# Optimization experiments

Measured on AMD Instinct MI355X. Metric: run time of the kernel, lower is better.

## Reference

```python
import jax, jax.numpy as jnp
import numpy as np

N = 100000   # nodes
E = 1600000  # edges (avg degree 16)
D = 64       # feature / hidden / embedding dim
OUT = 2
NEG_SLOPE = 0.2


def setup_inputs() -> dict:
    key = jax.random.key(0)
    ks = jax.random.split(key, 12)
    s = 1.0 / np.sqrt(D)
    return {
        "x": jax.random.normal(ks[0], (N, D), dtype=jnp.float32),
        "edge_index": jax.random.randint(ks[1], (2, E), 0, N, dtype=jnp.int64),
        "Wl": jax.random.normal(ks[2], (3, D, D), dtype=jnp.float32) * s,
        "bl": jnp.zeros((3, D), dtype=jnp.float32),
        "Wr": jax.random.normal(ks[3], (3, D, D), dtype=jnp.float32) * s,
        "br": jnp.zeros((3, D), dtype=jnp.float32),
        "att": jax.random.normal(ks[4], (3, D), dtype=jnp.float32) * s,
        "bg": jnp.zeros((3, D), dtype=jnp.float32),
        "Ws": jax.random.normal(ks[5], (3, D, D), dtype=jnp.float32) * s,
        "bs": jnp.zeros((3, D), dtype=jnp.float32),
        "Wout": jax.random.normal(ks[6], (D, OUT), dtype=jnp.float32) * s,
        "bout": jnp.zeros((OUT,), dtype=jnp.float32),
    }


def _gatv2(h, src, dst, Wl, bl, Wr, br, att, bg):
    # GATv2Conv (heads=1, concat, add_self_loops=False):
    #   e_ij = att . LeakyReLU(Wl h_j + Wr h_i); softmax over incoming edges of i;
    #   out_i = sum_j alpha_ij * (Wl h_j) + bias
    xl = h @ Wl + bl                      # [N, D] source transform
    xr = h @ Wr + br                      # [N, D] dest transform
    e = jax.nn.leaky_relu(xl[src] + xr[dst], NEG_SLOPE) @ att  # [E]
    m = jax.ops.segment_max(e, dst, num_segments=N)            # per-dest max
    a = jnp.exp(e - m[dst])                                    # [E]
    denom = jax.ops.segment_sum(a, dst, num_segments=N)        # [N]
    alpha = a / denom[dst]                                     # [E]
    agg = jax.ops.segment_sum(alpha[:, None] * xl[src], dst, num_segments=N)
    return agg + bg                                            # [N, D]


def reference(x, edge_index, Wl, bl, Wr, br, att, bg, Ws, bs, Wout, bout):
    src, dst = edge_index[0], edge_index[1]
    # layer 1: gat1 + skip1, relu (dropout_rate=0 -> identity)
    h = jax.nn.relu(_gatv2(x, src, dst, Wl[0], bl[0], Wr[0], br[0], att[0], bg[0])
                    + x @ Ws[0] + bs[0])
    # middle layer
    h = jax.nn.relu(_gatv2(h, src, dst, Wl[1], bl[1], Wr[1], br[1], att[1], bg[1])
                    + h @ Ws[1] + bs[1])
    # last gat layer: no relu after
    h = _gatv2(h, src, dst, Wl[2], bl[2], Wr[2], br[2], att[2], bg[2]) + h @ Ws[2] + bs[2]
    return h @ Wout + bout
```

## Files before the change

kernel.cpp:

```cpp
#include <hip/hip_runtime.h>
#include <stdint.h>

#define NN 100000
#define EE 1600000
#define DD 64
#define NBUCK 391
#define SCWG 200
#define SCCHUNK 8000

using short8 = __attribute__((ext_vector_type(8))) short;
using f32x4  = __attribute__((ext_vector_type(4))) float;
using f2     = __attribute__((ext_vector_type(2))) float;


__device__ __forceinline__ unsigned short bf16_rne(float f) {
    unsigned int u = __float_as_uint(f);
    unsigned int r = (u + 0x7FFFu + ((u >> 16) & 1u)) >> 16;
    return (unsigned short)r;
}
__device__ __forceinline__ float bf16_to_f32(unsigned short h) {
    return __uint_as_float(((unsigned int)h) << 16);
}


__global__ void bucket_hist(const int* __restrict__ dst, int* __restrict__ bhist) {
    __shared__ int h[NBUCK];
    int t = threadIdx.x;
    for (int b = t; b < NBUCK; b += 256) h[b] = 0;
    __syncthreads();
    int start = blockIdx.x * SCCHUNK;
    int endi = min(start + SCCHUNK, EE);
    for (int e = start + t; e < endi; e += 256)
        atomicAdd(&h[dst[e] >> 8], 1);
    __syncthreads();
    for (int b = t; b < NBUCK; b += 256)
        if (h[b]) atomicAdd(&bhist[b], h[b]);
}

__global__ void bucket_scan(const int* __restrict__ bhist, int* __restrict__ bbase,
                            int* __restrict__ bcursor, int* __restrict__ offsets) {
    __shared__ int s[512];
    int t = threadIdx.x;
    int v = (t < NBUCK) ? bhist[t] : 0;
    s[t] = v;
    __syncthreads();
    for (int off = 1; off < 512; off <<= 1) {
        int a = (t >= off) ? s[t - off] : 0;
        __syncthreads();
        s[t] += a;
        __syncthreads();
    }
    if (t < NBUCK) { int excl = s[t] - v; bbase[t] = excl; bcursor[t] = excl; }
    if (t == 0) { bbase[NBUCK] = EE; offsets[NN] = EE; }
}

__global__ void bucket_scatter(const int* __restrict__ src, const int* __restrict__ dst,
                               int* __restrict__ bcursor, unsigned int* __restrict__ bedges) {
    __shared__ int cnt[NBUCK];
    __shared__ int lcur[NBUCK];
    int t = threadIdx.x;
    for (int b = t; b < NBUCK; b += 256) cnt[b] = 0;
    __syncthreads();
    int start = blockIdx.x * SCCHUNK;
    int endi = min(start + SCCHUNK, EE);
    for (int e = start + t; e < endi; e += 256)
        atomicAdd(&cnt[dst[e] >> 8], 1);
    __syncthreads();
    for (int b = t; b < NBUCK; b += 256) {
        int c = cnt[b];
        lcur[b] = c ? atomicAdd(&bcursor[b], c) : 0;
    }
    __syncthreads();
    for (int e = start + t; e < endi; e += 256) {
        int d = dst[e];
        int pos = atomicAdd(&lcur[d >> 8], 1);
        bedges[pos] = ((unsigned int)(d & 255) << 24) | (unsigned int)src[e];
    }
}

__global__ void bucket_csr(const unsigned int* __restrict__ bedges, const int* __restrict__ bbase,
                           int* __restrict__ offsets, int* __restrict__ csr) {
    __shared__ int ncnt[256];
    __shared__ int lofs[256];
    int b = blockIdx.x;
    int t = threadIdx.x;
    int beg = bbase[b], endb = bbase[b + 1];
    ncnt[t] = 0;
    __syncthreads();
    for (int e = beg + t; e < endb; e += 256)
        atomicAdd(&ncnt[bedges[e] >> 24], 1);
    __syncthreads();
    int v = ncnt[t];
    lofs[t] = v;
    __syncthreads();
    for (int off = 1; off < 256; off <<= 1) {
        int a = (t >= off) ? lofs[t - off] : 0;
        __syncthreads();
        lofs[t] += a;
        __syncthreads();
    }
    int excl = lofs[t] - v;
    int node = b * 256 + t;
    if (node < NN) offsets[node] = beg + excl;
    __syncthreads();
    ncnt[t] = beg + excl;
    __syncthreads();
    for (int e = beg + t; e < endb; e += 256) {
        unsigned int ed = bedges[e];
        int pos = atomicAdd(&ncnt[ed >> 24], 1);
        csr[pos] = (int)(ed & 0xFFFFFFu);
    }
}


__global__ void conv_w(const float* __restrict__ Wl, const float* __restrict__ Wr,
                       const float* __restrict__ Ws,
                       unsigned short* __restrict__ Wt_hi, unsigned short* __restrict__ Wt_lo) {
    int e = blockIdx.x * 256 + threadIdx.x;
    if (e >= 9 * 4096) return;
    int mat = e >> 12;
    int r   = e & 4095;
    int k   = r >> 6, n = r & 63;
    int L = mat / 3, j = mat % 3;
    const float* W = (j == 0) ? Wl : ((j == 1) ? Wr : Ws);
    float v = W[L * 4096 + k * 64 + n];
    unsigned short hi = bf16_rne(v);
    unsigned short lo = bf16_rne(v - bf16_to_f32(hi));
    Wt_hi[mat * 4096 + n * 64 + k] = hi;
    Wt_lo[mat * 4096 + n * 64 + k] = lo;
}


__global__ void conv_x(const float* __restrict__ x,
                       unsigned short* __restrict__ Ahi, unsigned short* __restrict__ Alo) {
    int i = blockIdx.x * 256 + threadIdx.x;
    int total = NN * 16;
    for (; i < total; i += gridDim.x * 256) {
        float4 v = *(const float4*)&x[(size_t)i * 4];
        ushort4 h, l;
        h.x = bf16_rne(v.x); l.x = bf16_rne(v.x - bf16_to_f32(h.x));
        h.y = bf16_rne(v.y); l.y = bf16_rne(v.y - bf16_to_f32(h.y));
        h.z = bf16_rne(v.z); l.z = bf16_rne(v.z - bf16_to_f32(h.z));
        h.w = bf16_rne(v.w); l.w = bf16_rne(v.w - bf16_to_f32(h.w));
        *(ushort4*)&Ahi[(size_t)i * 4] = h;
        *(ushort4*)&Alo[(size_t)i * 4] = l;
    }
}


__global__ __launch_bounds__(256) void gemm_mfma(
    const unsigned short* __restrict__ Ahi, const unsigned short* __restrict__ Alo,
    const unsigned short* __restrict__ Wt_hi, const unsigned short* __restrict__ Wt_lo,
    const float* __restrict__ bl, const float* __restrict__ br, const float* __restrict__ bs,
    unsigned short* __restrict__ Xlb, float* __restrict__ XRS) {
    int lane = threadIdx.x & 63;
    int wid  = threadIdx.x >> 6;
    int m0 = (blockIdx.x * 4 + wid) * 16;
    if (m0 >= NN) return;

    int arow = m0 + (lane & 15);
    if (arow >= NN) arow = NN - 1;
    int koff = (lane >> 4) * 8;

    const unsigned short* abase = Ahi + (size_t)arow * 64;
    const unsigned short* lbase = Alo + (size_t)arow * 64;
    short8 ahi0 = *(const short8*)(abase + koff);
    short8 ahi1 = *(const short8*)(abase + 32 + koff);
    short8 alo0 = *(const short8*)(lbase + koff);
    short8 alo1 = *(const short8*)(lbase + 32 + koff);

    int col16 = lane & 15;
    int r0 = m0 + ((lane >> 4) << 2);

#pragma unroll
    for (int m = 0; m < 3; m++) {
        const unsigned short* wh = Wt_hi + m * 4096;
        const unsigned short* wl = Wt_lo + m * 4096;
        const float* bias = (m == 0) ? bl : ((m == 1) ? br : bs);
#pragma unroll
        for (int tt = 0; tt < 4; tt++) {
            int ncol = tt * 16 + col16;
            const unsigned short* bh = wh + ncol * 64 + koff;
            const unsigned short* blo = wl + ncol * 64 + koff;
            short8 bhi0 = *(const short8*)bh;
            short8 bhi1 = *(const short8*)(bh + 32);
            short8 blo0 = *(const short8*)blo;
            short8 blo1 = *(const short8*)(blo + 32);

            f32x4 acc = {0.f, 0.f, 0.f, 0.f};
            acc = __builtin_amdgcn_mfma_f32_16x16x32_bf16(ahi0, bhi0, acc, 0, 0, 0);
            acc = __builtin_amdgcn_mfma_f32_16x16x32_bf16(ahi1, bhi1, acc, 0, 0, 0);
            acc = __builtin_amdgcn_mfma_f32_16x16x32_bf16(ahi0, blo0, acc, 0, 0, 0);
            acc = __builtin_amdgcn_mfma_f32_16x16x32_bf16(ahi1, blo1, acc, 0, 0, 0);
            acc = __builtin_amdgcn_mfma_f32_16x16x32_bf16(alo0, bhi0, acc, 0, 0, 0);
            acc = __builtin_amdgcn_mfma_f32_16x16x32_bf16(alo1, bhi1, acc, 0, 0, 0);

            float bb = bias[ncol];
#pragma unroll
            for (int j = 0; j < 4; j++) {
                int row = r0 + j;
                if (row < NN) {
                    float v = acc[j] + bb;
                    if (m == 0)      Xlb[(size_t)row * 64 + ncol]       = bf16_rne(v);
                    else if (m == 1) XRS[(size_t)row * 128 + ncol]      = v;
                    else             XRS[(size_t)row * 128 + 64 + ncol] = v;
                }
            }
        }
    }
}


__device__ __forceinline__ float group_sum16(float t) {
    t += __int_as_float(__builtin_amdgcn_update_dpp(0, __float_as_int(t), 0xB1, 0xF, 0xF, true));
    t += __int_as_float(__builtin_amdgcn_update_dpp(0, __float_as_int(t), 0x4E, 0xF, 0xF, true));
    t += __int_as_float(__builtin_amdgcn_update_dpp(0, __float_as_int(t), 0x141, 0xF, 0xF, true));
    t += __int_as_float(__builtin_amdgcn_update_dpp(0, __float_as_int(t), 0x140, 0xF, 0xF, true));
    return t;
}

__global__ __launch_bounds__(256) void node_kernel(
    const unsigned short* __restrict__ Xlb, const float* __restrict__ XRS,
    const int* __restrict__ offsets, const int* __restrict__ csr,
    const float* __restrict__ att, const float* __restrict__ bg,
    unsigned short* __restrict__ houtHi, unsigned short* __restrict__ houtLo, int do_relu,
    const float* __restrict__ Wout, const float* __restrict__ bout,
    float* __restrict__ outp, int do_out) {
    int lane = threadIdx.x & 63;
    int wid  = threadIdx.x >> 6;
    int i = blockIdx.x * 4 + wid;
    if (i >= NN) return;
    int sub = lane & 15;
    int grp = lane >> 4;

    float4 xr4  = *(const float4*)&XRS[(size_t)i * 128 + sub * 4];
    float4 att4 = *(const float4*)&att[sub * 4];
    f2 xr01 = {xr4.x, xr4.y}, xr23 = {xr4.z, xr4.w};
    f2 at01 = {att4.x, att4.y}, at23 = {att4.z, att4.w};

    f2 agg01 = {0.f, 0.f}, agg23 = {0.f, 0.f};
    float denom = 0.f;
    int beg = offsets[i], end = offsets[i + 1];

    for (int j0 = beg; j0 < end; j0 += 8) {
        int jA = j0 + grp, jB = j0 + grp + 4;
        bool vA = jA < end, vB = jB < end;
        int sA = csr[vA ? jA : beg];
        int sB = csr[vB ? jB : beg];
        uint2 uA = *(const uint2*)&Xlb[(size_t)sA * 64 + sub * 4];
        uint2 uB = *(const uint2*)&Xlb[(size_t)sB * 64 + sub * 4];
        f2 xA01 = { __uint_as_float(uA.x << 16), __uint_as_float(uA.x & 0xFFFF0000u) };
        f2 xA23 = { __uint_as_float(uA.y << 16), __uint_as_float(uA.y & 0xFFFF0000u) };
        f2 xB01 = { __uint_as_float(uB.x << 16), __uint_as_float(uB.x & 0xFFFF0000u) };
        f2 xB23 = { __uint_as_float(uB.y << 16), __uint_as_float(uB.y & 0xFFFF0000u) };

        f2 sA01 = xA01 + xr01;
        f2 sA23 = xA23 + xr23;
        f2 sB01 = xB01 + xr01;
        f2 sB23 = xB23 + xr23;
        f2 lA01 = { fmaxf(sA01.x, 0.2f * sA01.x), fmaxf(sA01.y, 0.2f * sA01.y) };
        f2 lA23 = { fmaxf(sA23.x, 0.2f * sA23.x), fmaxf(sA23.y, 0.2f * sA23.y) };
        f2 lB01 = { fmaxf(sB01.x, 0.2f * sB01.x), fmaxf(sB01.y, 0.2f * sB01.y) };
        f2 lB23 = { fmaxf(sB23.x, 0.2f * sB23.x), fmaxf(sB23.y, 0.2f * sB23.y) };

        f2 tAv = lA01 * at01 + lA23 * at23;
        f2 tBv = lB01 * at01 + lB23 * at23;
        float tA = group_sum16(tAv.x + tAv.y);
        float tB = group_sum16(tBv.x + tBv.y);
        float aA = vA ? __expf(tA) : 0.f;
        float aB = vB ? __expf(tB) : 0.f;

        f2 aAv = {aA, aA};
        f2 aBv = {aB, aB};
        agg01 += aAv * xA01 + aBv * xB01;
        agg23 += aAv * xA23 + aBv * xB23;
        denom += aA + aB;
    }

    float aggx = agg01.x, aggy = agg01.y, aggz = agg23.x, aggw = agg23.y;
#pragma unroll
    for (int m = 16; m <= 32; m <<= 1) {
        aggx  += __shfl_xor(aggx, m, 64);
        aggy  += __shfl_xor(aggy, m, 64);
        aggz  += __shfl_xor(aggz, m, 64);
        aggw  += __shfl_xor(aggw, m, 64);
        denom += __shfl_xor(denom, m, 64);
    }

    float inv = (denom > 0.f) ? (1.0f / denom) : 0.f;
    float4 sk4 = *(const float4*)&XRS[(size_t)i * 128 + 64 + sub * 4];
    float4 bg4 = *(const float4*)&bg[sub * 4];
    float4 res;
    res.x = aggx * inv + bg4.x + sk4.x;
    res.y = aggy * inv + bg4.y + sk4.y;
    res.z = aggz * inv + bg4.z + sk4.z;
    res.w = aggw * inv + bg4.w + sk4.w;
    if (do_relu) {
        res.x = fmaxf(res.x, 0.f); res.y = fmaxf(res.y, 0.f);
        res.z = fmaxf(res.z, 0.f); res.w = fmaxf(res.w, 0.f);
    }
    if (do_out) {
        float4 w01 = *(const float4*)&Wout[8 * sub];
        float4 w23 = *(const float4*)&Wout[8 * sub + 4];
        float o0 = res.x * w01.x + res.y * w01.z + res.z * w23.x + res.w * w23.z;
        float o1 = res.x * w01.y + res.y * w01.w + res.z * w23.y + res.w * w23.w;
        o0 = group_sum16(o0);
        o1 = group_sum16(o1);
        if (lane == 0) {
            outp[(size_t)i * 2 + 0] = o0 + bout[0];
            outp[(size_t)i * 2 + 1] = o1 + bout[1];
        }
    } else {
        if (grp == 0) {
            ushort4 h, l;
            h.x = bf16_rne(res.x); l.x = bf16_rne(res.x - bf16_to_f32(h.x));
            h.y = bf16_rne(res.y); l.y = bf16_rne(res.y - bf16_to_f32(h.y));
            h.z = bf16_rne(res.z); l.z = bf16_rne(res.z - bf16_to_f32(h.z));
            h.w = bf16_rne(res.w); l.w = bf16_rne(res.w - bf16_to_f32(h.w));
            *(ushort4*)&houtHi[(size_t)i * 64 + sub * 4] = h;
            *(ushort4*)&houtLo[(size_t)i * 64 + sub * 4] = l;
        }
    }
}


extern "C" void kernel_launch(void* const* d_in, const int* in_sizes, int n_in,
                              void* d_out, int out_size, void* d_ws, size_t ws_size,
                              hipStream_t stream) {
    const float* x    = (const float*)d_in[0];
    const int*   ei   = (const int*)d_in[1];
    const float* Wl   = (const float*)d_in[2];
    const float* bl   = (const float*)d_in[3];
    const float* Wr   = (const float*)d_in[4];
    const float* br   = (const float*)d_in[5];
    const float* att  = (const float*)d_in[6];
    const float* bg   = (const float*)d_in[7];
    const float* Ws   = (const float*)d_in[8];
    const float* bs   = (const float*)d_in[9];
    const float* Wout = (const float*)d_in[10];
    const float* bout = (const float*)d_in[11];
    float* out = (float*)d_out;

    size_t off = 0;
    char* base = (char*)d_ws;
    auto alloc = [&](size_t bytes) -> void* {
        void* p = base + off;
        off += (bytes + 255) & ~(size_t)255;
        return p;
    };
    unsigned short* Xlb = (unsigned short*)alloc((size_t)NN * 64 * 2);
    float* XRS  = (float*)alloc((size_t)NN * 128 * 4);
    unsigned short* Ahi = (unsigned short*)alloc((size_t)NN * 64 * 2);
    unsigned short* Alo = (unsigned short*)alloc((size_t)NN * 64 * 2);
    unsigned short* Bhi = (unsigned short*)alloc((size_t)NN * 64 * 2);
    unsigned short* Blo = (unsigned short*)alloc((size_t)NN * 64 * 2);
    unsigned short* Wthi = (unsigned short*)alloc((size_t)9 * 4096 * 2);
    unsigned short* Wtlo = (unsigned short*)alloc((size_t)9 * 4096 * 2);
    int*  bhist  = (int*)alloc((size_t)NBUCK * 4);
    int*  bbase  = (int*)alloc((size_t)(NBUCK + 1) * 4);
    int*  bcur   = (int*)alloc((size_t)NBUCK * 4);
    unsigned int* bedges = (unsigned int*)alloc((size_t)EE * 4);
    int*  offs   = (int*)alloc((size_t)(NN + 1) * 4);
    int*  csr    = (int*)alloc((size_t)EE * 4);

    const int* src = ei;
    const int* dst = ei + EE;

    hipMemsetAsync(bhist, 0, (size_t)NBUCK * 4, stream);
    bucket_hist<<<SCWG, 256, 0, stream>>>(dst, bhist);
    bucket_scan<<<1, 512, 0, stream>>>(bhist, bbase, bcur, offs);
    bucket_scatter<<<SCWG, 256, 0, stream>>>(src, dst, bcur, bedges);
    bucket_csr<<<NBUCK, 256, 0, stream>>>(bedges, bbase, offs, csr);

    conv_w<<<(9 * 4096 + 255) / 256, 256, 0, stream>>>(Wl, Wr, Ws, Wthi, Wtlo);
    conv_x<<<2048, 256, 0, stream>>>(x, Ahi, Alo);

    unsigned short* curHi = Ahi; unsigned short* curLo = Alo;
    unsigned short* nxtHi = Bhi; unsigned short* nxtLo = Blo;
    for (int L = 0; L < 3; L++) {
        gemm_mfma<<<(NN + 63) / 64, 256, 0, stream>>>(
            curHi, curLo, Wthi + (size_t)L * 3 * 4096, Wtlo + (size_t)L * 3 * 4096,
            bl + L * 64, br + L * 64, bs + L * 64, Xlb, XRS);
        node_kernel<<<NN / 4, 256, 0, stream>>>(
            Xlb, XRS, offs, csr, att + L * 64, bg + L * 64,
            nxtHi, nxtLo, (L < 2) ? 1 : 0,
            Wout, bout, out, (L == 2) ? 1 : 0);
        unsigned short* th = curHi; curHi = nxtHi; nxtHi = th;
        unsigned short* tl = curLo; curLo = nxtLo; nxtLo = tl;
    }
}
```

Measured before the change: 382.2 us.

## Merge weight/input conversion kernels, transpose MFMA output for vector stores, use exp2

```diff
diff --git a/kernel.cpp b/kernel.cpp
--- a/kernel.cpp
+++ b/kernel.cpp
@@ -113,37 +113,37 @@
 }
 
 
-__global__ void conv_w(const float* __restrict__ Wl, const float* __restrict__ Wr,
-                       const float* __restrict__ Ws,
-                       unsigned short* __restrict__ Wt_hi, unsigned short* __restrict__ Wt_lo) {
-    int e = blockIdx.x * 256 + threadIdx.x;
-    if (e >= 9 * 4096) return;
-    int mat = e >> 12;
-    int r   = e & 4095;
-    int k   = r >> 6, n = r & 63;
-    int L = mat / 3, j = mat % 3;
-    const float* W = (j == 0) ? Wl : ((j == 1) ? Wr : Ws);
-    float v = W[L * 4096 + k * 64 + n];
-    unsigned short hi = bf16_rne(v);
-    unsigned short lo = bf16_rne(v - bf16_to_f32(hi));
-    Wt_hi[mat * 4096 + n * 64 + k] = hi;
-    Wt_lo[mat * 4096 + n * 64 + k] = lo;
-}
-
-
-__global__ void conv_x(const float* __restrict__ x,
-                       unsigned short* __restrict__ Ahi, unsigned short* __restrict__ Alo) {
-    int i = blockIdx.x * 256 + threadIdx.x;
-    int total = NN * 16;
-    for (; i < total; i += gridDim.x * 256) {
-        float4 v = *(const float4*)&x[(size_t)i * 4];
-        ushort4 h, l;
-        h.x = bf16_rne(v.x); l.x = bf16_rne(v.x - bf16_to_f32(h.x));
-        h.y = bf16_rne(v.y); l.y = bf16_rne(v.y - bf16_to_f32(h.y));
-        h.z = bf16_rne(v.z); l.z = bf16_rne(v.z - bf16_to_f32(h.z));
-        h.w = bf16_rne(v.w); l.w = bf16_rne(v.w - bf16_to_f32(h.w));
-        *(ushort4*)&Ahi[(size_t)i * 4] = h;
-        *(ushort4*)&Alo[(size_t)i * 4] = l;
+__global__ void conv_wx(const float* __restrict__ Wl, const float* __restrict__ Wr,
+                        const float* __restrict__ Ws, const float* __restrict__ x,
+                        unsigned short* __restrict__ Wt_hi, unsigned short* __restrict__ Wt_lo,
+                        unsigned short* __restrict__ Ahi, unsigned short* __restrict__ Alo) {
+    if (blockIdx.x < 144) {
+        int e = blockIdx.x * 256 + threadIdx.x;
+        if (e >= 9 * 4096) return;
+        int mat = e >> 12;
+        int r   = e & 4095;
+        int k   = r >> 6, n = r & 63;
+        int L = mat / 3, j = mat % 3;
+        const float* W = (j == 0) ? Wl : ((j == 1) ? Wr : Ws);
+        float v = W[L * 4096 + k * 64 + n];
+        unsigned short hi = bf16_rne(v);
+        unsigned short lo = bf16_rne(v - bf16_to_f32(hi));
+        Wt_hi[mat * 4096 + n * 64 + k] = hi;
+        Wt_lo[mat * 4096 + n * 64 + k] = lo;
+    } else {
+        int i = (blockIdx.x - 144) * 256 + threadIdx.x;
+        int total = NN * 16;
+        int stride = (gridDim.x - 144) * 256;
+        for (; i < total; i += stride) {
+            float4 v = *(const float4*)&x[(size_t)i * 4];
+            ushort4 h, l;
+            h.x = bf16_rne(v.x); l.x = bf16_rne(v.x - bf16_to_f32(h.x));
+            h.y = bf16_rne(v.y); l.y = bf16_rne(v.y - bf16_to_f32(h.y));
+            h.z = bf16_rne(v.z); l.z = bf16_rne(v.z - bf16_to_f32(h.z));
+            h.w = bf16_rne(v.w); l.w = bf16_rne(v.w - bf16_to_f32(h.w));
+            *(ushort4*)&Ahi[(size_t)i * 4] = h;
+            *(ushort4*)&Alo[(size_t)i * 4] = l;
+        }
     }
 }
 
@@ -158,9 +158,13 @@
     int m0 = (blockIdx.x * 4 + wid) * 16;
     if (m0 >= NN) return;
 
-    int arow = m0 + (lane & 15);
-    if (arow >= NN) arow = NN - 1;
-    int koff = (lane >> 4) * 8;
+    int l4 = lane & 15;
+    int hi = lane >> 4;
+    int koff = hi * 8;
+
+    int arow = m0 + l4;
+    bool rowok = (arow < NN);
+    if (!rowok) arow = NN - 1;
 
     const unsigned short* abase = Ahi + (size_t)arow * 64;
     const unsigned short* lbase = Alo + (size_t)arow * 64;
@@ -169,8 +173,7 @@
     short8 alo0 = *(const short8*)(lbase + koff);
     short8 alo1 = *(const short8*)(lbase + 32 + koff);
 
-    int col16 = lane & 15;
-    int r0 = m0 + ((lane >> 4) << 2);
+    int nbase0 = hi * 4;
 
 #pragma unroll
     for (int m = 0; m < 3; m++) {
@@ -179,7 +182,7 @@
         const float* bias = (m == 0) ? bl : ((m == 1) ? br : bs);
 #pragma unroll
         for (int tt = 0; tt < 4; tt++) {
-            int ncol = tt * 16 + col16;
+            int ncol = tt * 16 + l4;
             const unsigned short* bh = wh + ncol * 64 + koff;
             const unsigned short* blo = wl + ncol * 64 + koff;
             short8 bhi0 = *(const short8*)bh;
@@ -188,22 +191,29 @@
             short8 blo1 = *(const short8*)(blo + 32);
 
             f32x4 acc = {0.f, 0.f, 0.f, 0.f};
-            acc = __builtin_amdgcn_mfma_f32_16x16x32_bf16(ahi0, bhi0, acc, 0, 0, 0);
-            acc = __builtin_amdgcn_mfma_f32_16x16x32_bf16(ahi1, bhi1, acc, 0, 0, 0);
-            acc = __builtin_amdgcn_mfma_f32_16x16x32_bf16(ahi0, blo0, acc, 0, 0, 0);
-            acc = __builtin_amdgcn_mfma_f32_16x16x32_bf16(ahi1, blo1, acc, 0, 0, 0);
-            acc = __builtin_amdgcn_mfma_f32_16x16x32_bf16(alo0, bhi0, acc, 0, 0, 0);
-            acc = __builtin_amdgcn_mfma_f32_16x16x32_bf16(alo1, bhi1, acc, 0, 0, 0);
-
-            float bb = bias[ncol];
-#pragma unroll
-            for (int j = 0; j < 4; j++) {
-                int row = r0 + j;
-                if (row < NN) {
-                    float v = acc[j] + bb;
-                    if (m == 0)      Xlb[(size_t)row * 64 + ncol]       = bf16_rne(v);
-                    else if (m == 1) XRS[(size_t)row * 128 + ncol]      = v;
-                    else             XRS[(size_t)row * 128 + 64 + ncol] = v;
+            acc = __builtin_amdgcn_mfma_f32_16x16x32_bf16(bhi0, ahi0, acc, 0, 0, 0);
+            acc = __builtin_amdgcn_mfma_f32_16x16x32_bf16(bhi1, ahi1, acc, 0, 0, 0);
+            acc = __builtin_amdgcn_mfma_f32_16x16x32_bf16(blo0, ahi0, acc, 0, 0, 0);
+            acc = __builtin_amdgcn_mfma_f32_16x16x32_bf16(blo1, ahi1, acc, 0, 0, 0);
+            acc = __builtin_amdgcn_mfma_f32_16x16x32_bf16(bhi0, alo0, acc, 0, 0, 0);
+            acc = __builtin_amdgcn_mfma_f32_16x16x32_bf16(bhi1, alo1, acc, 0, 0, 0);
+
+            int nb = tt * 16 + nbase0;
+            float4 bb = *(const float4*)&bias[nb];
+            if (rowok) {
+                if (m == 0) {
+                    ushort4 hh;
+                    hh.x = bf16_rne(acc[0] + bb.x);
+                    hh.y = bf16_rne(acc[1] + bb.y);
+                    hh.z = bf16_rne(acc[2] + bb.z);
+                    hh.w = bf16_rne(acc[3] + bb.w);
+                    *(ushort4*)&Xlb[(size_t)arow * 64 + nb] = hh;
+                } else {
+                    float4 vv;
+                    vv.x = acc[0] + bb.x; vv.y = acc[1] + bb.y;
+                    vv.z = acc[2] + bb.z; vv.w = acc[3] + bb.w;
+                    int coff = (m == 1) ? 0 : 64;
+                    *(float4*)&XRS[(size_t)arow * 128 + coff + nb] = vv;
                 }
             }
         }
@@ -235,8 +245,9 @@
 
     float4 xr4  = *(const float4*)&XRS[(size_t)i * 128 + sub * 4];
     float4 att4 = *(const float4*)&att[sub * 4];
+    const float LOG2E = 1.44269504088896340736f;
     f2 xr01 = {xr4.x, xr4.y}, xr23 = {xr4.z, xr4.w};
-    f2 at01 = {att4.x, att4.y}, at23 = {att4.z, att4.w};
+    f2 at01 = {att4.x * LOG2E, att4.y * LOG2E}, at23 = {att4.z * LOG2E, att4.w * LOG2E};
 
     f2 agg01 = {0.f, 0.f}, agg23 = {0.f, 0.f};
     float denom = 0.f;
@@ -267,8 +278,8 @@
         f2 tBv = lB01 * at01 + lB23 * at23;
         float tA = group_sum16(tAv.x + tAv.y);
         float tB = group_sum16(tBv.x + tBv.y);
-        float aA = vA ? __expf(tA) : 0.f;
-        float aB = vB ? __expf(tB) : 0.f;
+        float aA = vA ? exp2f(tA) : 0.f;
+        float aB = vB ? exp2f(tB) : 0.f;
 
         f2 aAv = {aA, aA};
         f2 aBv = {aB, aB};
@@ -372,8 +383,7 @@
     bucket_scatter<<<SCWG, 256, 0, stream>>>(src, dst, bcur, bedges);
     bucket_csr<<<NBUCK, 256, 0, stream>>>(bedges, bbase, offs, csr);
 
-    conv_w<<<(9 * 4096 + 255) / 256, 256, 0, stream>>>(Wl, Wr, Ws, Wthi, Wtlo);
-    conv_x<<<2048, 256, 0, stream>>>(x, Ahi, Alo);
+    conv_wx<<<144 + 400, 256, 0, stream>>>(Wl, Wr, Ws, x, Wthi, Wtlo, Ahi, Alo);
 
     unsigned short* curHi = Ahi; unsigned short* curLo = Alo;
     unsigned short* nxtHi = Bhi; unsigned short* nxtLo = Blo;
```

Measured after the change: 399.9 us. 4.6% more time.
